# Optimization experiments

Hardware: AMD Instinct MI355X
Metric: run time of the kernel (lower is better)

Reference implementation:

```python
import jax, jax.numpy as jnp
import numpy as np

K = 3
TOP_K = 10
MASK_RATIO = 0.5
EPS_COS = 1e-8
EPS_DEG = 1e-6


def setup_inputs() -> dict:
    key = jax.random.key(0)
    ks = jax.random.split(key, 10)
    N, C, H, O, E = 4096, 128, 128, 64, 65536
    x = jax.random.normal(ks[0], (N, C), dtype=jnp.float32)
    edge_index = jax.random.randint(ks[1], (2, E), 0, N, dtype=jnp.int64)
    alpha = jnp.full((K,), 1.0 / K, dtype=jnp.float32)
    fusion_W = 0.02 * jax.random.normal(ks[2], (2 * H, H), dtype=jnp.float32)
    fusion_b = jnp.zeros((H,), dtype=jnp.float32)
    lin0_W = 0.02 * jax.random.normal(ks[3], (C, H), dtype=jnp.float32)
    lin0_b = jnp.zeros((H,), dtype=jnp.float32)
    lin1_W = 0.02 * jax.random.normal(ks[4], (H, O), dtype=jnp.float32)
    lin1_b = jnp.zeros((O,), dtype=jnp.float32)
    return {
        "x": x, "edge_index": edge_index, "alpha": alpha,
        "fusion_W": fusion_W, "fusion_b": fusion_b,
        "lin0_W": lin0_W, "lin0_b": lin0_b,
        "lin1_W": lin1_W, "lin1_b": lin1_b,
    }


def reference(x, edge_index, alpha, fusion_W, fusion_b, lin0_W, lin0_b, lin1_W, lin1_b):
    N = x.shape[0]
    # dense adjacency and its powers: A^0 = I (so A^0 @ x = x), A^1, A^2
    A = jnp.zeros((N, N), x.dtype).at[edge_index[0], edge_index[1]].set(1.0)
    A2 = A @ A
    hop_feats = jnp.stack([x, A @ x, A2 @ x], axis=0)  # [K, N, C]

    # per-node cosine-similarity top-k (self always included, cos=1)
    xn = x / (jnp.linalg.norm(x, axis=-1, keepdims=True) + EPS_COS)
    sim = xn @ xn.T  # [N, N]
    _, topk_idx = jax.lax.top_k(sim, TOP_K)  # [N, TOP_K]

    # random keep-mask per node, forced True at top-k neighbors
    mask = jax.random.uniform(jax.random.key(42), (N, N)) < MASK_RATIO
    rows = jnp.arange(N)[:, None]
    mask = mask.at[rows, topk_idx].set(True)
    Mf = mask.astype(x.dtype)  # [N, N]

    # alpha-weighted multi-hop aggregate, masked mean over selected nodes
    agg = jnp.einsum('k,knc->nc', alpha, hop_feats)  # [N, C]
    fused = (Mf @ agg) / (Mf.sum(axis=1, keepdims=True) + EPS_DEG)  # [N, C]

    h = jnp.concatenate([x, fused], axis=-1) @ fusion_W + fusion_b
    h = jax.nn.relu(h @ lin0_W + lin0_b)  # dropout inactive in eval
    out = h @ lin1_W + lin1_b
    return jax.nn.log_softmax(out, axis=1)
```

## Files before the change

### kernel.cpp

```cpp
#include <hip/hip_runtime.h>
#include <hip/hip_bf16.h>
#include <stdint.h>


#define N_NODES 4096
#define C_DIM   128
#define WPR     128
#define HALF_P  8388608u
#define TOPK    10
#define LSTR    11
#define JSPLIT  4

typedef __attribute__((ext_vector_type(8))) short bf16x8;
typedef __attribute__((ext_vector_type(4))) float f32x4;

__device__ __forceinline__ uint16_t f2bf(float f) {
    uint32_t u = __float_as_uint(f);
    return (uint16_t)((u + 0x7FFFu + ((u >> 16) & 1u)) >> 16);
}

__device__ __forceinline__ uint32_t rotl32(uint32_t v, int r) {
    return (v << r) | (v >> (32 - r));
}

__device__ __forceinline__ void threefry2x32(uint32_t k0, uint32_t k1,
                                             uint32_t x0, uint32_t x1,
                                             uint32_t& o0, uint32_t& o1) {
    uint32_t ks2 = k0 ^ k1 ^ 0x1BD11BDAu;
    x0 += k0; x1 += k1;
#define TF_ROUND(r) { x0 += x1; x1 = rotl32(x1, (r)); x1 ^= x0; }
    TF_ROUND(13) TF_ROUND(15) TF_ROUND(26) TF_ROUND(6)
    x0 += k1;  x1 += ks2 + 1u;
    TF_ROUND(17) TF_ROUND(29) TF_ROUND(16) TF_ROUND(24)
    x0 += ks2; x1 += k0 + 2u;
    TF_ROUND(13) TF_ROUND(15) TF_ROUND(26) TF_ROUND(6)
    x0 += k0;  x1 += k1 + 3u;
    TF_ROUND(17) TF_ROUND(29) TF_ROUND(16) TF_ROUND(24)
    x0 += k1;  x1 += ks2 + 4u;
    TF_ROUND(13) TF_ROUND(15) TF_ROUND(26) TF_ROUND(6)
    x0 += ks2; x1 += k0 + 5u;
#undef TF_ROUND
    o0 = x0; o1 = x1;
}

__global__ void scatter_kernel(const int* __restrict__ ei, int E,
                               uint32_t* __restrict__ Abits) {
    __shared__ int cnt_oddnz;
    int t = threadIdx.x;
    if (t == 0) cnt_oddnz = 0;
    __syncthreads();
    if (((const uint32_t*)ei)[2 * t + 1] != 0u) atomicAdd(&cnt_oddnz, 1);
    __syncthreads();
    bool is64 = (cnt_oddnz <= 8);
    int e = blockIdx.x * blockDim.x + t;
    if (e >= E) return;
    int src, dst;
    if (is64) { src = ei[2 * e]; dst = ei[2 * (E + e)]; }
    else      { src = ei[e];     dst = ei[E + e]; }
    src &= (N_NODES - 1);
    dst &= (N_NODES - 1);
    atomicOr(&Abits[src * WPR + (dst >> 5)], 1u << (dst & 31));
}

__global__ void spmm_kernel(const uint32_t* __restrict__ Abits,
                            const float* __restrict__ in,
                            float* __restrict__ out) {
    int i = blockIdx.x;
    int c = threadIdx.x;
    __shared__ uint32_t wbits[WPR];
    wbits[c] = Abits[i * WPR + c];
    __syncthreads();
    float acc = 0.f;
    for (int w = 0; w < WPR; ++w) {
        uint32_t bits = wbits[w];
        while (bits) {
            int b = __ffs(bits) - 1;
            bits &= bits - 1;
            acc += in[(w * 32 + b) * C_DIM + c];
        }
    }
    out[i * C_DIM + c] = acc;
}

__global__ void spmm2_agg_kernel(const uint32_t* __restrict__ Abits,
                                 const float* __restrict__ hop1,
                                 const float* __restrict__ xf,
                                 const float* __restrict__ alpha,
                                 float* __restrict__ agg) {
    int i = blockIdx.x;
    int c = threadIdx.x;
    __shared__ uint32_t wbits[WPR];
    wbits[c] = Abits[i * WPR + c];
    __syncthreads();
    float acc = 0.f;
    for (int w = 0; w < WPR; ++w) {
        uint32_t bits = wbits[w];
        while (bits) {
            int b = __ffs(bits) - 1;
            bits &= bits - 1;
            acc += hop1[(w * 32 + b) * C_DIM + c];
        }
    }
    agg[i * C_DIM + c] = alpha[0] * xf[i * C_DIM + c]
                       + alpha[1] * hop1[i * C_DIM + c]
                       + alpha[2] * acc;
}

__global__ void norm_kernel(const float* __restrict__ xf,
                            uint16_t* __restrict__ xnb) {
    int i = blockIdx.x;
    int c = threadIdx.x;
    float v = xf[i * C_DIM + c];
    float sq = v * v;
    #pragma unroll
    for (int off = 32; off >= 1; off >>= 1) sq += __shfl_xor(sq, off);
    __shared__ float ws[2];
    if ((c & 63) == 0) ws[c >> 6] = sq;
    __syncthreads();
    float tot = ws[0] + ws[1];
    xnb[i * C_DIM + c] = f2bf(v / (sqrtf(tot) + 1e-8f));
}

__global__ void transpose_bf_kernel(const float* __restrict__ agg,
                                    uint16_t* __restrict__ aggTb) {
    __shared__ float tile[32][33];
    int bi = blockIdx.x;
    int bc = blockIdx.y;
    int tx = threadIdx.x & 31, ty = threadIdx.x >> 5;
    #pragma unroll
    for (int r = 0; r < 32; r += 8)
        tile[ty + r][tx] = agg[(size_t)(bi * 32 + ty + r) * C_DIM + bc * 32 + tx];
    __syncthreads();
    #pragma unroll
    for (int r = 0; r < 32; r += 8)
        aggTb[(size_t)(bc * 32 + ty + r) * N_NODES + bi * 32 + tx] =
            f2bf(tile[tx][ty + r]);
}

__global__ void mask_kernel(uint32_t* __restrict__ Mbits,
                            int* __restrict__ degpre) {
    uint32_t tid = blockIdx.x * blockDim.x + threadIdx.x;
    uint32_t base = tid * 32u;
    uint32_t w0 = 0u, w1 = 0u;
    for (int k = 0; k < 32; ++k) {
        uint32_t o0, o1;
        threefry2x32(0u, 42u, base + k, HALF_P + base + k, o0, o1);
        w0 |= (uint32_t)((o0 >> 31) ^ 1u) << k;
        w1 |= (uint32_t)((o1 >> 31) ^ 1u) << k;
    }
    Mbits[tid] = w0;
    Mbits[(HALF_P >> 5) + tid] = w1;
    int p0 = __popc(w0), p1 = __popc(w1);
    #pragma unroll
    for (int off = 32; off >= 1; off >>= 1) {
        p0 += __shfl_xor(p0, off);
        p1 += __shfl_xor(p1, off);
    }
    if ((threadIdx.x & 63) == 0) {
        int row0 = (int)(tid >> 7);
        atomicAdd(&degpre[row0], p0);
        atomicAdd(&degpre[2048 + row0], p1);
    }
}

__launch_bounds__(512, 3)
__global__ void topk_kernel(const uint16_t* __restrict__ xnb,
                            float* __restrict__ topv,
                            int* __restrict__ topi) {
    int i0 = blockIdx.x * 16;
    int part = blockIdx.y;
    int t = threadIdx.x;
    int w = t >> 6;
    int lane = t & 63;
    int col = lane & 15;
    int quad = lane >> 4;

    __shared__ float sval[16 * 32 * LSTR];
    __shared__ int   sidx[16 * 32 * LSTR];

    bf16x8 bfi[4];
    #pragma unroll
    for (int s = 0; s < 4; ++s)
        bfi[s] = *(const bf16x8*)&xnb[(size_t)(i0 + col) * C_DIM + s * 32 + quad * 8];

    float tv[TOPK]; int ti[TOPK];
    #pragma unroll
    for (int k = 0; k < TOPK; ++k) { tv[k] = -1e30f; ti[k] = 0x7fffffff; }

    int jt0 = part * 64 + w * 8;
    for (int p = 0; p < 4; ++p) {
        int j0a = (jt0 + 2 * p) * 16;
        int j0b = j0a + 16;
        f32x4 acc0 = {0.f, 0.f, 0.f, 0.f};
        f32x4 acc1 = {0.f, 0.f, 0.f, 0.f};
        #pragma unroll
        for (int s = 0; s < 4; ++s) {
            bf16x8 aj0 = *(const bf16x8*)&xnb[(size_t)(j0a + col) * C_DIM + s * 32 + quad * 8];
            bf16x8 aj1 = *(const bf16x8*)&xnb[(size_t)(j0b + col) * C_DIM + s * 32 + quad * 8];
            acc0 = __builtin_amdgcn_mfma_f32_16x16x32_bf16(aj0, bfi[s], acc0, 0, 0, 0);
            acc1 = __builtin_amdgcn_mfma_f32_16x16x32_bf16(aj1, bfi[s], acc1, 0, 0, 0);
        }
        #pragma unroll
        for (int g = 0; g < 2; ++g) {
            f32x4 acc = g ? acc1 : acc0;
            int j0 = g ? j0b : j0a;
            float m4 = fmaxf(fmaxf(acc[0], acc[1]), fmaxf(acc[2], acc[3]));
            if (m4 > tv[TOPK-1]) {
                #pragma unroll
                for (int r = 0; r < 4; ++r) {
                    float d = acc[r];
                    if (d > tv[TOPK-1]) {
                        int j = j0 + quad * 4 + r;
                        tv[TOPK-1] = d; ti[TOPK-1] = j;
                        #pragma unroll
                        for (int q = TOPK - 2; q >= 0; --q) {
                            if (tv[q+1] > tv[q]) {
                                float fv = tv[q]; tv[q] = tv[q+1]; tv[q+1] = fv;
                                int iv = ti[q];  ti[q] = ti[q+1];  ti[q+1] = iv;
                            }
                        }
                    }
                }
            }
        }
    }

    int base = (col * 32 + w * 4 + quad) * LSTR;
    #pragma unroll
    for (int k = 0; k < TOPK; ++k) { sval[base + k] = tv[k]; sidx[base + k] = ti[k]; }

    int row = t >> 5, L = t & 31;
    for (int s = 16; s >= 1; s >>= 1) {
        __syncthreads();
        if (L < s) {
            int la = (row * 32 + L) * LSTR;
            int lb = (row * 32 + L + s) * LSTR;
            float ov[TOPK]; int oi[TOPK];
            int ia = 0, ib = 0;
            #pragma unroll
            for (int k = 0; k < TOPK; ++k) {
                float va = sval[la + ia], vb = sval[lb + ib];
                int   xa = sidx[la + ia], xb = sidx[lb + ib];
                bool takeA = (va > vb) || (va == vb && xa < xb);
                if (takeA) { ov[k] = va; oi[k] = xa; ++ia; }
                else       { ov[k] = vb; oi[k] = xb; ++ib; }
            }
            #pragma unroll
            for (int k = 0; k < TOPK; ++k) { sval[la + k] = ov[k]; sidx[la + k] = oi[k]; }
        }
    }
    __syncthreads();
    if (t < 16) {
        size_t gi = (size_t)(part * N_NODES + i0 + t) * TOPK;
        #pragma unroll
        for (int k = 0; k < TOPK; ++k) {
            topv[gi + k] = sval[(t * 32) * LSTR + k];
            topi[gi + k] = sidx[(t * 32) * LSTR + k];
        }
    }
}

__global__ void topmerge_kernel(const float* __restrict__ topv,
                                const int* __restrict__ topi,
                                const int* __restrict__ degpre,
                                uint32_t* __restrict__ Mbits,
                                float* __restrict__ deg) {
    int i = blockIdx.x * blockDim.x + threadIdx.x;
    if (i >= N_NODES) return;
    const float* v[JSPLIT]; const int* x[JSPLIT]; int ix[JSPLIT];
    #pragma unroll
    for (int q = 0; q < JSPLIT; ++q) {
        v[q] = topv + (size_t)(q * N_NODES + i) * TOPK;
        x[q] = topi + (size_t)(q * N_NODES + i) * TOPK;
        ix[q] = 0;
    }
    int newc = 0;
    #pragma unroll
    for (int k = 0; k < TOPK; ++k) {
        float bestv = -1e38f; int bestj = 0x7fffffff; int bestq = 0;
        #pragma unroll
        for (int q = 0; q < JSPLIT; ++q) {
            bool ok = ix[q] < TOPK;
            float fv = ok ? v[q][ix[q]] : -1e38f;
            int   jj = ok ? x[q][ix[q]] : 0x7fffffff;
            if (fv > bestv || (fv == bestv && jj < bestj)) {
                bestv = fv; bestj = jj; bestq = q;
            }
        }
        ++ix[bestq];
        uint32_t* wp = &Mbits[(size_t)i * WPR + (bestj >> 5)];
        uint32_t old = *wp, bit = 1u << (bestj & 31);
        newc += ((old & bit) == 0u);
        *wp = old | bit;
    }
    deg[i] = (float)(degpre[i] + newc);
}

__launch_bounds__(512, 2)
__global__ void fused_kernel(const uint32_t* __restrict__ Mbits,
                             const uint16_t* __restrict__ aggTb,
                             float* __restrict__ fpart) {
    int i0 = blockIdx.x * 16;
    int part = blockIdx.y;
    int t = threadIdx.x;
    int w = t >> 6;
    int lane = t & 63;
    int col = lane & 15;
    int quad = lane >> 4;

    const uint32_t* mrow = Mbits + (size_t)(i0 + col) * WPR;
    const uint16_t* brow = aggTb + (size_t)(w * 16 + col) * N_NODES;
    f32x4 acc[4];
    #pragma unroll
    for (int u = 0; u < 4; ++u) acc[u] = (f32x4){0.f, 0.f, 0.f, 0.f};

    int kbase = part * 2048;
    for (int k0 = kbase; k0 < kbase + 2048; k0 += 128) {
        uint4 mw4 = *(const uint4*)&mrow[k0 >> 5];
        uint32_t mws[4] = {mw4.x, mw4.y, mw4.z, mw4.w};
        #pragma unroll
        for (int u = 0; u < 4; ++u) {
            uint32_t byte = (mws[u] >> (quad * 8)) & 0xFFu;
            union { uint32_t uu[4]; bf16x8 v; } a;
            #pragma unroll
            for (int pp = 0; pp < 4; ++pp) {
                uint32_t lo = (byte >> (2 * pp)) & 1u;
                uint32_t hi = (byte >> (2 * pp + 1)) & 1u;
                a.uu[pp] = (lo ? 0x3F80u : 0u) | (hi ? 0x3F800000u : 0u);
            }
            bf16x8 b = *(const bf16x8*)&brow[k0 + u * 32 + quad * 8];
            acc[u] = __builtin_amdgcn_mfma_f32_16x16x32_bf16(a.v, b, acc[u], 0, 0, 0);
        }
    }
    #pragma unroll
    for (int r = 0; r < 4; ++r) {
        int il = quad * 4 + r;
        float s = (acc[0][r] + acc[1][r]) + (acc[2][r] + acc[3][r]);
        fpart[(size_t)part * (N_NODES * C_DIM)
              + (size_t)(i0 + il) * C_DIM + w * 16 + col] = s;
    }
}

__global__ void mlp_kernel(const float* __restrict__ xf,
                           const float* __restrict__ fpart,
                           const float* __restrict__ deg,
                           const float* __restrict__ fW, const float* __restrict__ fB,
                           const float* __restrict__ l0W, const float* __restrict__ l0B,
                           const float* __restrict__ l1W, const float* __restrict__ l1B,
                           float* __restrict__ out) {
    int i0 = blockIdx.x * 4;
    int t = threadIdx.x;
    __shared__ float lx[4][256];
    __shared__ float hb[4][128];
    const float* f0 = fpart;
    const float* f1 = fpart + (size_t)N_NODES * C_DIM;
    for (int r = t; r < 4 * 128; r += 128) {
        int row = r >> 7, c = r & 127;
        size_t idx = (size_t)(i0 + row) * C_DIM + c;
        lx[row][c] = xf[idx];
        lx[row][128 + c] = (f0[idx] + f1[idx]) / (deg[i0 + row] + 1e-6f);
    }
    __syncthreads();
    float acc[4];
    #pragma unroll
    for (int r = 0; r < 4; ++r) acc[r] = fB[t];
    for (int k = 0; k < 256; ++k) {
        float wv = fW[k * 128 + t];
        #pragma unroll
        for (int r = 0; r < 4; ++r) acc[r] = fmaf(lx[r][k], wv, acc[r]);
    }
    #pragma unroll
    for (int r = 0; r < 4; ++r) hb[r][t] = acc[r];
    __syncthreads();
    #pragma unroll
    for (int r = 0; r < 4; ++r) acc[r] = l0B[t];
    for (int k = 0; k < 128; ++k) {
        float wv = l0W[k * 128 + t];
        #pragma unroll
        for (int r = 0; r < 4; ++r) acc[r] = fmaf(hb[r][k], wv, acc[r]);
    }
    __syncthreads();
    #pragma unroll
    for (int r = 0; r < 4; ++r) lx[r][t] = fmaxf(acc[r], 0.f);
    __syncthreads();
    int o = t & 63, pr = t >> 6;
    #pragma unroll
    for (int rr = 0; rr < 2; ++rr) {
        int r = pr + 2 * rr;
        float a = l1B[o];
        for (int k = 0; k < 128; ++k)
            a = fmaf(lx[r][k], l1W[k * 64 + o], a);
        float m = a;
        #pragma unroll
        for (int off = 32; off >= 1; off >>= 1) m = fmaxf(m, __shfl_xor(m, off));
        float e = expf(a - m);
        float s = e;
        #pragma unroll
        for (int off = 32; off >= 1; off >>= 1) s += __shfl_xor(s, off);
        out[(size_t)(i0 + r) * 64 + o] = a - m - logf(s);
    }
}

extern "C" void kernel_launch(void* const* d_in, const int* in_sizes, int n_in,
                              void* d_out, int out_size, void* d_ws, size_t ws_size,
                              hipStream_t stream) {
    const float* xf    = (const float*)d_in[0];
    const int*   ei    = (const int*)d_in[1];
    const float* alpha = (const float*)d_in[2];
    const float* fW    = (const float*)d_in[3];
    const float* fB    = (const float*)d_in[4];
    const float* l0W   = (const float*)d_in[5];
    const float* l0B   = (const float*)d_in[6];
    const float* l1W   = (const float*)d_in[7];
    const float* l1B   = (const float*)d_in[8];
    float* out = (float*)d_out;
    const int E  = in_sizes[1] / 2;
    const int NC = N_NODES * C_DIM;

    char* p = (char*)d_ws;
    const size_t SZ = (size_t)NC * 4;
    uint32_t* Abits  = (uint32_t*)p; p += SZ;
    int*      degpre = (int*)p;      p += N_NODES * 4;
    float*    hop1   = (float*)p;    p += SZ;
    float*    agg    = (float*)p;    p += SZ;
    uint32_t* Mbits  = (uint32_t*)p; p += SZ;
    float*    fpart  = (float*)p;    p += 2 * SZ;
    uint16_t* xnb    = (uint16_t*)p; p += SZ / 2;
    uint16_t* aggTb  = (uint16_t*)p; p += SZ / 2;
    float*    deg    = (float*)p;    p += N_NODES * 4;
    float*    topv   = (float*)p;    p += (size_t)JSPLIT * N_NODES * TOPK * 4;
    int*      topi   = (int*)p;      p += (size_t)JSPLIT * N_NODES * TOPK * 4;

    hipMemsetAsync(Abits, 0, SZ + N_NODES * 4, stream);
    scatter_kernel<<<(E + 255) / 256, 256, 0, stream>>>(ei, E, Abits);
    spmm_kernel<<<N_NODES, 128, 0, stream>>>(Abits, xf, hop1);
    spmm2_agg_kernel<<<N_NODES, 128, 0, stream>>>(Abits, hop1, xf, alpha, agg);
    norm_kernel<<<N_NODES, 128, 0, stream>>>(xf, xnb);
    transpose_bf_kernel<<<dim3(128, 4), 256, 0, stream>>>(agg, aggTb);
    mask_kernel<<<(HALF_P >> 5) / 256, 256, 0, stream>>>(Mbits, degpre);
    topk_kernel<<<dim3(N_NODES / 16, JSPLIT), 512, 0, stream>>>(xnb, topv, topi);
    topmerge_kernel<<<N_NODES / 256, 256, 0, stream>>>(topv, topi, degpre, Mbits, deg);
    fused_kernel<<<dim3(N_NODES / 16, 2), 512, 0, stream>>>(Mbits, aggTb, fpart);
    mlp_kernel<<<N_NODES / 4, 128, 0, stream>>>(xf, fpart, deg,
                                                fW, fB, l0W, l0B, l1W, l1B, out);
}
```

Baseline: 257.5 us.

## Shrink topk shared memory and registers, relayout merge buffers for occupancy

The topk kernel now stores candidate indices as 16-bit values, pads the shared stride to 13, and transposes the shared layout so the 16 rows interleave and merge lanes touch adjacent slots. It processes one 16-column tile per loop iteration instead of two, and raises the launch-bounds occupancy hint from 3 to 4 blocks. The aim is lower LDS and register use so more blocks fit per CU, with fewer bank conflicts in the tree merge. In exchange, each iteration has less MFMA instruction-level parallelism, and the tighter register budget could cause spills.

```diff
diff --git a/kernel.cpp b/kernel.cpp
--- a/kernel.cpp
+++ b/kernel.cpp
@@ -8,7 +8,7 @@
 #define WPR     128
 #define HALF_P  8388608u
 #define TOPK    10
-#define LSTR    11
+#define LSTR    13
 #define JSPLIT  4
 
 typedef __attribute__((ext_vector_type(8))) short bf16x8;
@@ -163,7 +163,7 @@
     }
 }
 
-__launch_bounds__(512, 3)
+__launch_bounds__(512, 4)
 __global__ void topk_kernel(const uint16_t* __restrict__ xnb,
                             float* __restrict__ topv,
                             int* __restrict__ topi) {
@@ -175,8 +175,8 @@
     int col = lane & 15;
     int quad = lane >> 4;
 
-    __shared__ float sval[16 * 32 * LSTR];
-    __shared__ int   sidx[16 * 32 * LSTR];
+    __shared__ float    sval[32 * 16 * LSTR];
+    __shared__ uint16_t sidx[32 * 16 * LSTR];
 
     bf16x8 bfi[4];
     #pragma unroll
@@ -185,39 +185,30 @@
 
     float tv[TOPK]; int ti[TOPK];
     #pragma unroll
-    for (int k = 0; k < TOPK; ++k) { tv[k] = -1e30f; ti[k] = 0x7fffffff; }
+    for (int k = 0; k < TOPK; ++k) { tv[k] = -1e30f; ti[k] = 0xFFFF; }
 
     int jt0 = part * 64 + w * 8;
-    for (int p = 0; p < 4; ++p) {
-        int j0a = (jt0 + 2 * p) * 16;
-        int j0b = j0a + 16;
-        f32x4 acc0 = {0.f, 0.f, 0.f, 0.f};
-        f32x4 acc1 = {0.f, 0.f, 0.f, 0.f};
+    for (int p = 0; p < 8; ++p) {
+        int j0 = (jt0 + p) * 16;
+        f32x4 acc = {0.f, 0.f, 0.f, 0.f};
         #pragma unroll
         for (int s = 0; s < 4; ++s) {
-            bf16x8 aj0 = *(const bf16x8*)&xnb[(size_t)(j0a + col) * C_DIM + s * 32 + quad * 8];
-            bf16x8 aj1 = *(const bf16x8*)&xnb[(size_t)(j0b + col) * C_DIM + s * 32 + quad * 8];
-            acc0 = __builtin_amdgcn_mfma_f32_16x16x32_bf16(aj0, bfi[s], acc0, 0, 0, 0);
-            acc1 = __builtin_amdgcn_mfma_f32_16x16x32_bf16(aj1, bfi[s], acc1, 0, 0, 0);
-        }
-        #pragma unroll
-        for (int g = 0; g < 2; ++g) {
-            f32x4 acc = g ? acc1 : acc0;
-            int j0 = g ? j0b : j0a;
-            float m4 = fmaxf(fmaxf(acc[0], acc[1]), fmaxf(acc[2], acc[3]));
-            if (m4 > tv[TOPK-1]) {
-                #pragma unroll
-                for (int r = 0; r < 4; ++r) {
-                    float d = acc[r];
-                    if (d > tv[TOPK-1]) {
-                        int j = j0 + quad * 4 + r;
-                        tv[TOPK-1] = d; ti[TOPK-1] = j;
-                        #pragma unroll
-                        for (int q = TOPK - 2; q >= 0; --q) {
-                            if (tv[q+1] > tv[q]) {
-                                float fv = tv[q]; tv[q] = tv[q+1]; tv[q+1] = fv;
-                                int iv = ti[q];  ti[q] = ti[q+1];  ti[q+1] = iv;
-                            }
+            bf16x8 aj = *(const bf16x8*)&xnb[(size_t)(j0 + col) * C_DIM + s * 32 + quad * 8];
+            acc = __builtin_amdgcn_mfma_f32_16x16x32_bf16(aj, bfi[s], acc, 0, 0, 0);
+        }
+        float m4 = fmaxf(fmaxf(acc[0], acc[1]), fmaxf(acc[2], acc[3]));
+        if (m4 > tv[TOPK-1]) {
+            #pragma unroll
+            for (int r = 0; r < 4; ++r) {
+                float d = acc[r];
+                if (d > tv[TOPK-1]) {
+                    int j = j0 + quad * 4 + r;
+                    tv[TOPK-1] = d; ti[TOPK-1] = j;
+                    #pragma unroll
+                    for (int q = TOPK - 2; q >= 0; --q) {
+                        if (tv[q+1] > tv[q]) {
+                            float fv = tv[q]; tv[q] = tv[q+1]; tv[q+1] = fv;
+                            int iv = ti[q];  ti[q] = ti[q+1];  ti[q+1] = iv;
                         }
                     }
                 }
@@ -225,22 +216,25 @@
         }
     }
 
-    int base = (col * 32 + w * 4 + quad) * LSTR;
-    #pragma unroll
-    for (int k = 0; k < TOPK; ++k) { sval[base + k] = tv[k]; sidx[base + k] = ti[k]; }
-
-    int row = t >> 5, L = t & 31;
+    int base = ((w * 4 + quad) * 16 + col) * LSTR;
+    #pragma unroll
+    for (int k = 0; k < TOPK; ++k) {
+        sval[base + k] = tv[k];
+        sidx[base + k] = (uint16_t)ti[k];
+    }
+
+    int row = t & 15, L = t >> 4;
     for (int s = 16; s >= 1; s >>= 1) {
         __syncthreads();
         if (L < s) {
-            int la = (row * 32 + L) * LSTR;
-            int lb = (row * 32 + L + s) * LSTR;
-            float ov[TOPK]; int oi[TOPK];
+            int la = (L * 16 + row) * LSTR;
+            int lb = ((L + s) * 16 + row) * LSTR;
+            float ov[TOPK]; uint16_t oi[TOPK];
             int ia = 0, ib = 0;
             #pragma unroll
             for (int k = 0; k < TOPK; ++k) {
                 float va = sval[la + ia], vb = sval[lb + ib];
-                int   xa = sidx[la + ia], xb = sidx[lb + ib];
+                uint16_t xa = sidx[la + ia], xb = sidx[lb + ib];
                 bool takeA = (va > vb) || (va == vb && xa < xb);
                 if (takeA) { ov[k] = va; oi[k] = xa; ++ia; }
                 else       { ov[k] = vb; oi[k] = xb; ++ib; }
@@ -254,8 +248,8 @@
         size_t gi = (size_t)(part * N_NODES + i0 + t) * TOPK;
         #pragma unroll
         for (int k = 0; k < TOPK; ++k) {
-            topv[gi + k] = sval[(t * 32) * LSTR + k];
-            topi[gi + k] = sidx[(t * 32) * LSTR + k];
+            topv[gi + k] = sval[t * LSTR + k];
+            topi[gi + k] = (int)sidx[t * LSTR + k];
         }
     }
 }
```

Result: faster. 250.7 us (-2.7%).
